# Optimization experiments

Hardware: AMD Instinct MI355X
Metric: run time of the kernel (lower is better)

## Reference

```python
import jax, jax.numpy as jnp
import numpy as np

L_BBOX, L_GIOU, L_OBJ, AUX_W = 5.0, 2.0, 1.0, 0.5
EPS = 1e-7


def _xyxy(b):
    # cxcywh -> xyxy
    return jnp.concatenate([b[..., :2] - b[..., 2:] * 0.5,
                            b[..., :2] + b[..., 2:] * 0.5], axis=-1)


def _giou(a, b):
    # a, b: [..., 4] xyxy (broadcastable) -> giou [...]
    area_a = (a[..., 2] - a[..., 0]) * (a[..., 3] - a[..., 1])
    area_b = (b[..., 2] - b[..., 0]) * (b[..., 3] - b[..., 1])
    lt = jnp.maximum(a[..., :2], b[..., :2])
    rb = jnp.minimum(a[..., 2:], b[..., 2:])
    wh = jnp.maximum(rb - lt, 0.0)
    inter = wh[..., 0] * wh[..., 1]
    union = area_a + area_b - inter
    iou = inter / (union + EPS)
    lte = jnp.minimum(a[..., :2], b[..., :2])
    rbe = jnp.maximum(a[..., 2:], b[..., 2:])
    whe = jnp.maximum(rbe - lte, 0.0)
    enc = whe[..., 0] * whe[..., 1]
    return iou - (enc - union) / (enc + EPS)


def _bce_sum(logits, targets):
    # numerically stable BCE-with-logits, reduction='sum'
    return jnp.sum(jnp.maximum(logits, 0.0) - logits * targets
                   + jnp.log1p(jnp.exp(-jnp.abs(logits))))


def _hungarian(cost):
    # exact Kuhn-Munkres (shortest augmenting path), rectangular, minimization
    cost = np.asarray(cost, dtype=np.float64)
    transposed = cost.shape[0] > cost.shape[1]
    if transposed:
        cost = cost.T
    n, m = cost.shape
    u = np.zeros(n + 1)
    v = np.zeros(m + 1)
    p = np.zeros(m + 1, dtype=np.int64)
    way = np.zeros(m + 1, dtype=np.int64)
    for i in range(1, n + 1):
        p[0] = i
        j0 = 0
        minv = np.full(m + 1, np.inf)
        used = np.zeros(m + 1, dtype=bool)
        while True:
            used[j0] = True
            i0 = p[j0]
            cur = cost[i0 - 1] - u[i0] - v[1:]
            free = ~used[1:]
            better = free & (cur < minv[1:])
            minv[1:] = np.where(better, cur, minv[1:])
            way[1:] = np.where(better, j0, way[1:])
            free_idx = np.nonzero(free)[0]
            jbest = free_idx[np.argmin(minv[1:][free_idx])]
            delta = minv[1 + jbest]
            u[p[used]] += delta
            v[used] -= delta
            minv[~used] -= delta
            j0 = jbest + 1
            if p[j0] == 0:
                break
        while j0:
            j1 = way[j0]
            p[j0] = p[j1]
            j0 = j1
    rows = p[1:] - 1
    cols = np.nonzero(rows >= 0)[0]
    rows = rows[cols]
    if transposed:
        rows, cols = cols, rows
    return rows.astype(np.int64), cols.astype(np.int64)


def _match(pred_bboxes, target_bboxes, bbox_mask):
    # batched cost matrix built on-device, Hungarian per sample (no_grad path)
    pxy = _xyxy(pred_bboxes)
    txy = _xyxy(target_bboxes)
    c_l1 = jnp.sum(jnp.abs(pred_bboxes[:, :, None, :] - target_bboxes[:, None, :, :]), -1)
    c_giou = -_giou(pxy[:, :, None, :], txy[:, None, :, :])
    C = np.asarray(L_BBOX * c_l1 + L_GIOU * c_giou)        # [B,N,M]
    mask = np.asarray(bbox_mask)
    B, N, M = C.shape
    pidx = np.zeros((B, M), np.int32)
    tidx = np.zeros((B, M), np.int32)
    pm = np.zeros((B, M), np.float32)
    for i in range(B):
        vid = np.nonzero(mask[i] > 0.5)[0]
        k = vid.size
        if k == 0:
            continue
        r, c = _hungarian(C[i][:, vid])
        pidx[i, :k] = r
        tidx[i, :k] = vid[c]
        pm[i, :k] = 1.0
    return jnp.asarray(pidx), jnp.asarray(tidx), jnp.asarray(pm)


def _det_losses(pred_bboxes, obj_logits, target_bboxes, pidx, tidx, pm):
    B, N = pred_bboxes.shape[:2]
    bi = jnp.arange(B)[:, None]
    mp = pred_bboxes[bi, pidx]               # [B,M,4] matched preds (padded)
    mt = target_bboxes[bi, tidx]             # [B,M,4] matched targets
    nb = jnp.maximum(pm.sum(), 1.0)
    bbox_loss = (jnp.abs(mp - mt).sum(-1) * pm).sum() / nb
    giou_loss = ((1.0 - _giou(_xyxy(mp), _xyxy(mt))) * pm).sum() / nb
    obj_t = jnp.zeros((B, N), pred_bboxes.dtype).at[bi, pidx].max(pm)
    obj_loss = _bce_sum(obj_logits[..., 0], obj_t) / (B * N)
    return bbox_loss, giou_loss, obj_loss, obj_t


def _total(cls_logits, label, pred_bboxes, obj_scores, target_bboxes,
           aux_pred_bboxes, aux_obj_scores, pidx, tidx, pm):
    B = cls_logits.shape[0]
    cls_loss = -jax.nn.log_softmax(cls_logits, -1)[jnp.arange(B), label].mean()
    bbox_loss, giou_loss, obj_loss, obj_t = _det_losses(
        pred_bboxes, obj_scores, target_bboxes, pidx, tidx, pm)
    # aux losses, vectorized over L decoder layers
    L = aux_pred_bboxes.shape[0]
    bi = jnp.arange(B)[:, None]
    mpa = aux_pred_bboxes[:, bi, pidx]                      # [L,B,M,4]
    mt = target_bboxes[bi, tidx][None]                      # [1,B,M,4]
    nb = jnp.maximum(pm.sum(), 1.0)
    aux_bbox = (jnp.abs(mpa - mt).sum(-1) * pm[None]).sum() / nb
    aux_giou = ((1.0 - _giou(_xyxy(mpa), _xyxy(mt))) * pm[None]).sum() / nb
    N = pred_bboxes.shape[1]
    aux_obj = _bce_sum(aux_obj_scores[..., 0], obj_t[None]) / (B * N)
    aux_loss = (L_BBOX * aux_bbox + L_GIOU * aux_giou + L_OBJ * aux_obj) * AUX_W / L
    return (cls_loss + L_BBOX * bbox_loss + L_GIOU * giou_loss
            + L_OBJ * obj_loss + aux_loss)


def setup_inputs() -> dict:
    B, N, M, L, C = 32, 300, 60, 5, 1000
    ks = jax.random.split(jax.random.key(0), 9)
    cls_logits = jax.random.normal(ks[0], (B, C), jnp.float32)
    label = jax.random.randint(ks[1], (B,), 0, C)
    pred_bboxes = jax.random.uniform(ks[2], (B, N, 4), jnp.float32)
    obj_scores = jax.random.normal(ks[3], (B, N, 1), jnp.float32)
    cxcy = jax.random.uniform(ks[4], (B, M, 2), jnp.float32, 0.2, 0.8)
    wh = jax.random.uniform(ks[5], (B, M, 2), jnp.float32, 0.05, 0.35)
    target_bboxes = jnp.concatenate([cxcy, wh], -1)
    counts = jax.random.randint(ks[6], (B,), 1, M + 1)
    bbox_mask = (jnp.arange(M)[None, :] < counts[:, None]).astype(jnp.float32)
    aux_pred_bboxes = jax.random.uniform(ks[7], (L, B, N, 4), jnp.float32)
    aux_obj_scores = jax.random.normal(ks[8], (L, B, N, 1), jnp.float32)
    return {"cls_logits": cls_logits, "label": label,
            "pred_bboxes": pred_bboxes, "obj_scores": obj_scores,
            "target_bboxes": target_bboxes, "bbox_mask": bbox_mask,
            "aux_pred_bboxes": aux_pred_bboxes,
            "aux_obj_scores": aux_obj_scores}


def reference(cls_logits, label, pred_bboxes, obj_scores, target_bboxes,
              bbox_mask, aux_pred_bboxes, aux_obj_scores):
    pidx, tidx, pm = _match(pred_bboxes, target_bboxes, bbox_mask)
    return _total(cls_logits, label, pred_bboxes, obj_scores, target_bboxes,
                  aux_pred_bboxes, aux_obj_scores, pidx, tidx, pm)
```

## Files before the change

### kernel.cpp

```cpp
#include <hip/hip_runtime.h>
#include <math.h>

#define BN   32
#define NN   300
#define MM   60
#define LAUX 5
#define CNUM 1000

#define LC_ROWS 53
#define CINF 3.0e38f

#define THR_ROW   1.5f
#define EXB_BATCH 3.0f

#define ACC_CLS   0
#define ACC_OBJ   1
#define ACC_AOBJ  2
#define ACC_BBOX  3
#define ACC_GIOU  4
#define ACC_ABBOX 5
#define ACC_AGIOU 6
#define ACC_NB    7

__device__ float  g_cost[BN * MM * NN + 64];
__device__ double g_acc[8];

__device__ __forceinline__ float giou_box(float ax0, float ay0, float ax1, float ay1,
                                          float bx0, float by0, float bx1, float by1) {
    const float EPS = 1e-7f;
    float area_a = (ax1 - ax0) * (ay1 - ay0);
    float area_b = (bx1 - bx0) * (by1 - by0);
    float ltx = fmaxf(ax0, bx0), lty = fmaxf(ay0, by0);
    float rbx = fminf(ax1, bx1), rby = fminf(ay1, by1);
    float w = fmaxf(rbx - ltx, 0.0f), h = fmaxf(rby - lty, 0.0f);
    float inter = w * h;
    float uni = area_a + area_b - inter;
    float iou = inter / (uni + EPS);
    float ex0 = fminf(ax0, bx0), ey0 = fminf(ay0, by0);
    float ex1 = fmaxf(ax1, bx1), ey1 = fmaxf(ay1, by1);
    float ew = fmaxf(ex1 - ex0, 0.0f), eh = fmaxf(ey1 - ey0, 0.0f);
    float enc = ew * eh;
    return iou - (enc - uni) / (enc + EPS);
}

__device__ __forceinline__ float pair_terms(float4 p, float tx0, float ty0,
                                            float tx1, float ty1,
                                            float t0, float t1, float t2, float t3,
                                            float* gi_out) {
    float l1 = fabsf(p.x - t0) + fabsf(p.y - t1) + fabsf(p.z - t2) + fabsf(p.w - t3);
    *gi_out = giou_box(p.x - p.z * 0.5f, p.y - p.w * 0.5f,
                       p.x + p.z * 0.5f, p.y + p.w * 0.5f, tx0, ty0, tx1, ty1);
    return l1;
}


__device__ __forceinline__ unsigned enc_key(float x, int col) {
    unsigned u = __float_as_uint(x);
    unsigned e = (u & 0x80000000u) ? ~u : (u | 0x80000000u);
    return (e & 0xFFFFFE00u) | (unsigned)col;
}
__device__ __forceinline__ float dec_key(unsigned kk) {
    unsigned e = kk & 0xFFFFFE00u;
    unsigned u = (e & 0x80000000u) ? (e & 0x7FFFFFFFu) : ~e;
    return __uint_as_float(u);
}

__device__ __forceinline__ unsigned wave_min_u32(unsigned k) {
#define WSTEP(C) { unsigned t = (unsigned)__builtin_amdgcn_update_dpp((int)k, (int)k, (C), 0xF, 0xF, false); \
                   k = (t < k) ? t : k; }
    WSTEP(0x111) WSTEP(0x112) WSTEP(0x114) WSTEP(0x118) WSTEP(0x142) WSTEP(0x143)
#undef WSTEP
    return (unsigned)__builtin_amdgcn_readlane((int)k, 63);
}

__device__ __forceinline__ void wave_min_pair(unsigned& a, unsigned& b) {
#define PSTEP(C) { \
    unsigned ta = (unsigned)__builtin_amdgcn_update_dpp((int)a, (int)a, (C), 0xF, 0xF, false); \
    unsigned tb = (unsigned)__builtin_amdgcn_update_dpp((int)b, (int)b, (C), 0xF, 0xF, false); \
    a = (ta < a) ? ta : a; \
    b = (tb < b) ? tb : b; }
    PSTEP(0x111) PSTEP(0x112) PSTEP(0x114) PSTEP(0x118) PSTEP(0x142) PSTEP(0x143)
#undef PSTEP
    a = (unsigned)__builtin_amdgcn_readlane((int)a, 63);
    b = (unsigned)__builtin_amdgcn_readlane((int)b, 63);
}

__device__ __forceinline__ void wave_min2_u32(unsigned& a1, unsigned& a2) {
#define W2STEP(C) { \
    unsigned b1 = (unsigned)__builtin_amdgcn_update_dpp(-1, (int)a1, (C), 0xF, 0xF, false); \
    unsigned b2 = (unsigned)__builtin_amdgcn_update_dpp(-1, (int)a2, (C), 0xF, 0xF, false); \
    unsigned lo = (b1 < a1) ? b1 : a1; \
    unsigned hi = (b1 < a1) ? a1 : b1; \
    unsigned mn = (b2 < a2) ? b2 : a2; \
    a2 = (hi < mn) ? hi : mn; \
    a1 = lo; }
    W2STEP(0x111) W2STEP(0x112) W2STEP(0x114) W2STEP(0x118) W2STEP(0x142) W2STEP(0x143)
#undef W2STEP
    a1 = (unsigned)__builtin_amdgcn_readlane((int)a1, 63);
    a2 = (unsigned)__builtin_amdgcn_readlane((int)a2, 63);
}

__device__ __forceinline__ int sel5i(const int* a, int s) {
    int r = a[0];
    r = (s == 1) ? a[1] : r;
    r = (s == 2) ? a[2] : r;
    r = (s == 3) ? a[3] : r;
    r = (s == 4) ? a[4] : r;
    return r;
}
__device__ __forceinline__ float sel5f(const float* a, int s) {
    float r = a[0];
    r = (s == 1) ? a[1] : r;
    r = (s == 2) ? a[2] : r;
    r = (s == 3) ? a[3] : r;
    r = (s == 4) ? a[4] : r;
    return r;
}
__device__ __forceinline__ int rdlane_i(int x, int l) { return __builtin_amdgcn_readlane(x, l); }
__device__ __forceinline__ float rdlane_f(float x, int l) {
    return __uint_as_float((unsigned)__builtin_amdgcn_readlane(__float_as_int(x), l));
}


__global__ __launch_bounds__(256) void fused_kernel(
    const float* __restrict__ mask, const float* __restrict__ pred,
    const float* __restrict__ tgt, const float* __restrict__ obj,
    const float* __restrict__ auxobj, const float* __restrict__ auxp,
    const float* __restrict__ logits, const int* __restrict__ label)
{
    const int b = blockIdx.x;
    const int tid = threadIdx.x;
    const int lane = tid & 63;
    const int wid = tid >> 6;

    __shared__ __align__(16) float lc[LC_ROWS * NN + 24];
    __shared__ int    claimc[NN];
    __shared__ double wred[28];
    __shared__ float  wmax[4];

    const float* pb = pred + (size_t)b * NN * 4;
    const float* tb = tgt + (size_t)b * MM * 4;
    float* gq = g_cost + (size_t)b * (MM * NN);

    for (int e = tid; e < MM * NN; e += 256) {
        int m = e / NN, n = e - m * NN;
        float4 p = *(const float4*)(pb + n * 4);
        float4 t = *(const float4*)(tb + m * 4);
        float l1 = fabsf(p.x - t.x) + fabsf(p.y - t.y) + fabsf(p.z - t.z) + fabsf(p.w - t.w);
        float gi = giou_box(p.x - p.z * 0.5f, p.y - p.w * 0.5f, p.x + p.z * 0.5f, p.y + p.w * 0.5f,
                            t.x - t.z * 0.5f, t.y - t.w * 0.5f, t.x + t.z * 0.5f, t.y + t.w * 0.5f);
        float cst = 5.0f * l1 - 2.0f * gi;
        if (m < LC_ROWS) lc[e] = cst; else gq[e] = cst;
    }
    for (int c = tid; c < NN; c += 256) claimc[c] = 0x7FFFFFFF;

    double so = 0.0, sa = 0.0;
    for (int i = tid; i < NN; i += 256) {
        float x = obj[(size_t)b * NN + i];
        so += (double)(fmaxf(x, 0.0f) + log1pf(expf(-fabsf(x))));
    }
    for (int i = tid; i < LAUX * NN; i += 256) {
        int l = i / NN, n = i - l * NN;
        float x = auxobj[((size_t)l * BN + b) * NN + n];
        sa += (double)(fmaxf(x, 0.0f) + log1pf(expf(-fabsf(x))));
    }
    const float* lrow = logits + (size_t)b * CNUM;
    float mx = -1e30f;
    for (int c = tid; c < CNUM; c += 256) mx = fmaxf(mx, lrow[c]);
    for (int off = 32; off; off >>= 1) mx = fmaxf(mx, __shfl_down(mx, off, 64));
    if (lane == 0) wmax[wid] = mx;
    __syncthreads();
    mx = fmaxf(fmaxf(wmax[0], wmax[1]), fmaxf(wmax[2], wmax[3]));
    double se = 0.0;
    for (int c = tid; c < CNUM; c += 256) se += exp((double)(lrow[c] - mx));
    for (int off = 32; off; off >>= 1) {
        so += __shfl_down(so, off, 64);
        sa += __shfl_down(sa, off, 64);
        se += __shfl_down(se, off, 64);
    }
    if (lane == 0) { wred[wid * 3] = so; wred[wid * 3 + 1] = sa; wred[wid * 3 + 2] = se; }
    __syncthreads();
    if (tid == 0) {
        double soT = wred[0] + wred[3] + wred[6] + wred[9];
        double saT = wred[1] + wred[4] + wred[7] + wred[10];
        double seT = wred[2] + wred[5] + wred[8] + wred[11];
        atomicAdd(&g_acc[ACC_OBJ], soT);
        atomicAdd(&g_acc[ACC_AOBJ], saT);
        atomicAdd(&g_acc[ACC_CLS], log(seT) + (double)mx - (double)lrow[label[b]]);
    }

#define LOAD_ROW(rv, ri) do { int _r = (ri); \
    if (_r < LC_ROWS) { const int _o = _r * NN + lane; \
        rv[0] = lc[_o]; rv[1] = lc[_o + 64]; rv[2] = lc[_o + 128]; \
        rv[3] = lc[_o + 192]; rv[4] = lc[_o + 256]; \
    } else { const float* _g = gq + (size_t)_r * NN + lane; \
        rv[0] = _g[0]; rv[1] = _g[64]; rv[2] = _g[128]; \
        rv[3] = _g[192]; rv[4] = _g[256]; } } while (0)

    float mval = (lane < MM) ? mask[b * MM + lane] : 0.0f;
    int k = __popcll(__ballot(mval > 0.5f));

    float v[5], minv[5], uc[5];
    int pc[5], way[5];
    int used_inv = 0;
#pragma unroll
    for (int s = 0; s < 5; s++) {
        v[s] = 0.0f; uc[s] = 0.0f; pc[s] = 0; way[s] = 0; minv[s] = CINF;
        if (s * 64 + lane >= NN) used_inv |= 1 << s;
    }

    unsigned rowkey = 0xFFFFFFFFu;
    if (wid == 0 && lane < k) {
        unsigned best = 0xFFFFFFFFu;
        if (lane < LC_ROWS) {
            const float* rp = lc + lane * NN;
            for (int c = 0; c < NN; c += 4) {
                float4 q = *(const float4*)(rp + c);
                unsigned c0 = enc_key(q.x, c);
                unsigned c1 = enc_key(q.y, c + 1);
                unsigned c2 = enc_key(q.z, c + 2);
                unsigned c3 = enc_key(q.w, c + 3);
                unsigned m01 = (c0 < c1) ? c0 : c1;
                unsigned m23 = (c2 < c3) ? c2 : c3;
                unsigned m = (m01 < m23) ? m01 : m23;
                best = (m < best) ? m : best;
            }
        } else {
            const float* rp = gq + (size_t)lane * NN;
            for (int c = 0; c < NN; c += 4) {
                float4 q = *(const float4*)(rp + c);
                unsigned c0 = enc_key(q.x, c);
                unsigned c1 = enc_key(q.y, c + 1);
                unsigned c2 = enc_key(q.z, c + 2);
                unsigned c3 = enc_key(q.w, c + 3);
                unsigned m01 = (c0 < c1) ? c0 : c1;
                unsigned m23 = (c2 < c3) ? c2 : c3;
                unsigned m = (m01 < m23) ? m01 : m23;
                best = (m < best) ? m : best;
            }
        }
        rowkey = best;
    }
    float u_row = dec_key(rowkey);
    int jr = (int)(rowkey & 0x1FFu);
    if (wid == 0 && lane < k) atomicMin(&claimc[jr], lane);
    __syncthreads();

    if (wid == 0) {
        unsigned long long assigned;
        {
            int jrs = (lane < k) ? jr : 0;
            bool won = (lane < k) && (claimc[jrs] == lane);
            assigned = __ballot(won);
        }
#pragma unroll
        for (int s = 0; s < 5; s++) {
            int c = s * 64 + lane;
            int w = (c < NN) ? claimc[c] : 0x7FFFFFFF;
            bool hit = (w != 0x7FFFFFFF);
            int wm = hit ? w : 0;
            unsigned kw = (unsigned)__builtin_amdgcn_ds_bpermute(wm << 2, (int)rowkey);
            float uw = dec_key(kw);
            pc[s] = hit ? (w + 1) : pc[s];
            uc[s] = hit ? uw : uc[s];
        }

        unsigned long long kmask = (k >= 64) ? ~0ull : ((1ull << k) - 1ull);
        unsigned long long pool = ~assigned & kmask;
        unsigned long long leftover = 0ull;
        {
            unsigned long long once = 0ull, twice = 0ull;
            int guard = 0;
            while (pool && guard++ < 4 * MM + 16) {
                int r = (int)__builtin_ctzll(pool);
                pool &= pool - 1;
                if ((twice >> r) & 1ull) { leftover |= 1ull << r; continue; }
                if ((once >> r) & 1ull) twice |= 1ull << r; else once |= 1ull << r;

                float rv[5];
                LOAD_ROW(rv, r);
                unsigned k1 = 0xFFFFFFFFu, k2 = 0xFFFFFFFFu;
#pragma unroll
                for (int s = 0; s < 5; s++) {
                    int c = s * 64 + lane;
                    unsigned kk = ((used_inv >> s) & 1) ? 0xFFFFFFFFu : enc_key(rv[s] - v[s], c);
                    unsigned lo = (kk < k1) ? kk : k1;
                    unsigned hi = (kk < k1) ? k1 : kk;
                    k2 = (hi < k2) ? hi : k2;
                    k1 = lo;
                }
                wave_min2_u32(k1, k2);
                float m1 = dec_key(k1), m2 = dec_key(k2);
                int j1 = (int)(k1 & 0x1FFu);
                int sl = j1 >> 6, ow = j1 & 63;
                int pj = rdlane_i(sel5i(pc, sl), ow);
                float dv = m2 - m1;
                u_row = (lane == r) ? m2 : u_row;
#pragma unroll
                for (int s = 0; s < 5; s++) {
                    bool hit = (lane == ow) && (s == sl);
                    v[s]  = hit ? v[s] - dv : v[s];
                    pc[s] = hit ? r + 1    : pc[s];
                    uc[s] = hit ? m2       : uc[s];
                }
                if (pj > 0) pool |= 1ull << (pj - 1);
            }
            leftover |= pool;
        }

        float exb = EXB_BATCH;
        while (leftover) {
            int r = (int)__builtin_ctzll(leftover);
            leftover &= leftover - 1;

            {
                float rv[5];
                LOAD_ROW(rv, r);
                unsigned kAll = 0xFFFFFFFFu, kFree = 0xFFFFFFFFu;
#pragma unroll
                for (int s = 0; s < 5; s++) {
                    int c = s * 64 + lane;
                    bool valid = !((used_inv >> s) & 1);
                    unsigned kk = valid ? enc_key(rv[s] - v[s], c) : 0xFFFFFFFFu;
                    kAll = (kk < kAll) ? kk : kAll;
                    unsigned kf = (valid && pc[s] == 0) ? kk : 0xFFFFFFFFu;
                    kFree = (kf < kFree) ? kf : kFree;
                }
                wave_min_pair(kAll, kFree);
                float m1 = dec_key(kAll), mf = dec_key(kFree);
                float spend = mf - m1;
                if (spend <= fminf(THR_ROW, exb)) {
                    exb -= spend;
                    int jf = (int)(kFree & 0x1FFu);
                    int slf = jf >> 6, owf = jf & 63;
                    u_row = (lane == r) ? m1 : u_row;
#pragma unroll
                    for (int s = 0; s < 5; s++) {
                        bool hit = (lane == owf) && (s == slf);
                        pc[s] = hit ? r + 1 : pc[s];
                        uc[s] = hit ? m1    : uc[s];
                    }
                    continue;
                }
            }

            int used = used_inv;
#pragma unroll
            for (int s = 0; s < 5; s++) minv[s] = CINF;
            float u_cur = rdlane_f(u_row, r);
            float u_i0 = u_cur;
            int i0 = r + 1;
            int j0 = 0;

            for (int guard = 0; guard < NN + 4; guard++) {
                if (j0 > 0) {
                    int c0 = j0 - 1, ow0 = c0 & 63, sl0 = c0 >> 6;
                    used |= (lane == ow0) ? (1 << sl0) : 0;
                }
                float rv[5];
                LOAD_ROW(rv, i0 - 1);
                unsigned kbest = 0xFFFFFFFFu;
#pragma unroll
                for (int s = 0; s < 5; s++) {
                    int c = s * 64 + lane;
                    bool skip = (used >> s) & 1;
                    float cur = rv[s] - u_i0 - v[s];
                    bool lt = !skip && (cur < minv[s]);
                    minv[s] = lt ? cur : minv[s];
                    way[s]  = lt ? j0 : way[s];
                    unsigned kk = skip ? 0xFFFFFFFFu : enc_key(minv[s], c);
                    kbest = (kk < kbest) ? kk : kbest;
                }
                unsigned kmin = wave_min_u32(kbest);
                float delta = dec_key(kmin);
                int jb = (int)(kmin & 0x1FFu);

                int sl = jb >> 6, ow = jb & 63;
                int pj = rdlane_i(sel5i(pc, sl), ow);
                float uj = rdlane_f(sel5f(uc, sl), ow);

                u_cur += delta;
#pragma unroll
                for (int s = 0; s < 5; s++) {
                    bool us = (used >> s) & 1;
                    v[s]    = us ? v[s] - delta   : v[s];
                    uc[s]   = us ? uc[s] + delta  : uc[s];
                    minv[s] = us ? minv[s]        : minv[s] - delta;
                }

                j0 = jb + 1;
                if (pj == 0) break;
                i0 = pj;
                u_i0 = uj;
            }

            int j = j0;
            int safety = 0;
            while (j && safety++ < NN + 4) {
                int co = j - 1, ow = co & 63, sl = co >> 6;
                int j1 = rdlane_i(sel5i(way, sl), ow);
                int pnew; float unew;
                if (j1 == 0) { pnew = r + 1; unew = u_cur; }
                else {
                    int co1 = j1 - 1, ow1 = co1 & 63, sl1 = co1 >> 6;
                    pnew = rdlane_i(sel5i(pc, sl1), ow1);
                    unew = rdlane_f(sel5f(uc, sl1), ow1);
                }
#pragma unroll
                for (int s = 0; s < 5; s++) {
                    bool hit = (lane == ow) && (s == sl);
                    pc[s] = hit ? pnew : pc[s];
                    uc[s] = hit ? unew : uc[s];
                }
                j = j1;
            }
        }

#pragma unroll
        for (int s = 0; s < 5; s++) {
            int c = s * 64 + lane;
            if (c < NN) claimc[c] = pc[s] - 1;
        }
    }
    __syncthreads();
#undef LOAD_ROW

    {
        double sb = 0.0, sg = 0.0, sab = 0.0, sag = 0.0, nb = 0.0;
        double som = 0.0, saom = 0.0;
        for (int it = tid; it < NN * (1 + LAUX); it += 256) {
            int l = it / NN, c = it - l * NN;
            int t = claimc[c];
            if (t >= 0) {
                float4 tg = *(const float4*)(tb + t * 4);
                float tx0 = tg.x - tg.z * 0.5f, ty0 = tg.y - tg.w * 0.5f;
                float tx1 = tg.x + tg.z * 0.5f, ty1 = tg.y + tg.w * 0.5f;
                if (l == 0) {
                    float4 p = *(const float4*)(pb + c * 4);
                    float gi;
                    float l1 = pair_terms(p, tx0, ty0, tx1, ty1, tg.x, tg.y, tg.z, tg.w, &gi);
                    sb += (double)l1;
                    sg += (double)(1.0f - gi);
                    nb += 1.0;
                    som += (double)obj[(size_t)b * NN + c];
                } else {
                    int la = l - 1;
                    float4 a = *(const float4*)(auxp + (((size_t)la * BN + b) * NN + c) * 4);
                    float gi;
                    float l1 = pair_terms(a, tx0, ty0, tx1, ty1, tg.x, tg.y, tg.z, tg.w, &gi);
                    sab += (double)l1;
                    sag += (double)(1.0f - gi);
                    saom += (double)auxobj[((size_t)la * BN + b) * NN + c];
                }
            }
        }
        for (int off = 32; off; off >>= 1) {
            sb   += __shfl_down(sb, off, 64);
            sg   += __shfl_down(sg, off, 64);
            sab  += __shfl_down(sab, off, 64);
            sag  += __shfl_down(sag, off, 64);
            nb   += __shfl_down(nb, off, 64);
            som  += __shfl_down(som, off, 64);
            saom += __shfl_down(saom, off, 64);
        }
        if (lane == 0) {
            double* wr = wred + wid * 7;
            wr[0] = sb; wr[1] = sg; wr[2] = sab; wr[3] = sag;
            wr[4] = nb; wr[5] = som; wr[6] = saom;
        }
        __syncthreads();
        if (tid == 0) {
            double tb0 = wred[0] + wred[7] + wred[14] + wred[21];
            double tg0 = wred[1] + wred[8] + wred[15] + wred[22];
            double tab = wred[2] + wred[9] + wred[16] + wred[23];
            double tag = wred[3] + wred[10] + wred[17] + wred[24];
            double tnb = wred[4] + wred[11] + wred[18] + wred[25];
            double tom = wred[5] + wred[12] + wred[19] + wred[26];
            double tam = wred[6] + wred[13] + wred[20] + wred[27];
            atomicAdd(&g_acc[ACC_BBOX], tb0);
            atomicAdd(&g_acc[ACC_GIOU], tg0);
            atomicAdd(&g_acc[ACC_ABBOX], tab);
            atomicAdd(&g_acc[ACC_AGIOU], tag);
            atomicAdd(&g_acc[ACC_NB], tnb);
            atomicAdd(&g_acc[ACC_OBJ], -tom);
            atomicAdd(&g_acc[ACC_AOBJ], -tam);
        }
    }
}

__global__ void final_kernel(float* __restrict__ out) {
    if (threadIdx.x == 0 && blockIdx.x == 0) {
        double nb = g_acc[ACC_NB];
        if (nb < 1.0) nb = 1.0;
        double cls = g_acc[ACC_CLS] / (double)BN;
        double bbox = g_acc[ACC_BBOX] / nb;
        double giou = g_acc[ACC_GIOU] / nb;
        double obj = g_acc[ACC_OBJ] / (double)(BN * NN);
        double ab = g_acc[ACC_ABBOX] / nb;
        double ag = g_acc[ACC_AGIOU] / nb;
        double ao = g_acc[ACC_AOBJ] / (double)(BN * NN);
        double aux = (5.0 * ab + 2.0 * ag + 1.0 * ao) * 0.5 / (double)LAUX;
        out[0] = (float)(cls + 5.0 * bbox + 2.0 * giou + obj + aux);
        for (int i = 0; i < 8; i++) g_acc[i] = 0.0;
    }
}

extern "C" void kernel_launch(void* const* d_in, const int* in_sizes, int n_in,
                              void* d_out, int out_size, void* d_ws, size_t ws_size,
                              hipStream_t stream) {
    const float* cls_logits = (const float*)d_in[0];
    const int* label = (const int*)d_in[1];
    const float* pred_bboxes = (const float*)d_in[2];
    const float* obj_scores = (const float*)d_in[3];
    const float* target_bboxes = (const float*)d_in[4];
    const float* bbox_mask = (const float*)d_in[5];
    const float* aux_pred = (const float*)d_in[6];
    const float* aux_obj = (const float*)d_in[7];
    float* out = (float*)d_out;

    fused_kernel<<<BN, 256, 0, stream>>>(bbox_mask, pred_bboxes, target_bboxes,
                                         obj_scores, aux_obj, aux_pred,
                                         cls_logits, label);
    final_kernel<<<1, 1, 0, stream>>>(out);
}
```

Baseline: 230.5 us.

## Keep full cost matrix in LDS and fold final reduction into main kernel

Enlarges the shared-memory cost buffer to hold all 60 target rows, removing the global-memory spill for the rows past 53 and the branch in every row load of the assignment loop. It also drops the separate finalize kernel: a global done counter lets the last block compute the output and reset the accumulators. This trades a larger LDS allocation and extra atomics for fewer global reads and one less launch.

```diff
diff --git a/kernel.cpp b/kernel.cpp
--- a/kernel.cpp
+++ b/kernel.cpp
@@ -7,7 +7,6 @@
 #define LAUX 5
 #define CNUM 1000
 
-#define LC_ROWS 53
 #define CINF 3.0e38f
 
 #define THR_ROW   1.5f
@@ -22,8 +21,8 @@
 #define ACC_AGIOU 6
 #define ACC_NB    7
 
-__device__ float  g_cost[BN * MM * NN + 64];
-__device__ double g_acc[8];
+__device__ double   g_acc[8];
+__device__ unsigned g_done = 0;
 
 __device__ __forceinline__ float giou_box(float ax0, float ay0, float ax1, float ay1,
                                           float bx0, float by0, float bx1, float by1) {
@@ -126,21 +125,21 @@
     const float* __restrict__ mask, const float* __restrict__ pred,
     const float* __restrict__ tgt, const float* __restrict__ obj,
     const float* __restrict__ auxobj, const float* __restrict__ auxp,
-    const float* __restrict__ logits, const int* __restrict__ label)
+    const float* __restrict__ logits, const int* __restrict__ label,
+    float* __restrict__ out)
 {
     const int b = blockIdx.x;
     const int tid = threadIdx.x;
     const int lane = tid & 63;
     const int wid = tid >> 6;
 
-    __shared__ __align__(16) float lc[LC_ROWS * NN + 24];
+    __shared__ __align__(16) float lc[MM * NN + 24];
     __shared__ int    claimc[NN];
     __shared__ double wred[28];
     __shared__ float  wmax[4];
 
     const float* pb = pred + (size_t)b * NN * 4;
     const float* tb = tgt + (size_t)b * MM * 4;
-    float* gq = g_cost + (size_t)b * (MM * NN);
 
     for (int e = tid; e < MM * NN; e += 256) {
         int m = e / NN, n = e - m * NN;
@@ -149,8 +148,7 @@
         float l1 = fabsf(p.x - t.x) + fabsf(p.y - t.y) + fabsf(p.z - t.z) + fabsf(p.w - t.w);
         float gi = giou_box(p.x - p.z * 0.5f, p.y - p.w * 0.5f, p.x + p.z * 0.5f, p.y + p.w * 0.5f,
                             t.x - t.z * 0.5f, t.y - t.w * 0.5f, t.x + t.z * 0.5f, t.y + t.w * 0.5f);
-        float cst = 5.0f * l1 - 2.0f * gi;
-        if (m < LC_ROWS) lc[e] = cst; else gq[e] = cst;
+        lc[e] = 5.0f * l1 - 2.0f * gi;
     }
     for (int c = tid; c < NN; c += 256) claimc[c] = 0x7FFFFFFF;
 
@@ -189,13 +187,9 @@
         atomicAdd(&g_acc[ACC_CLS], log(seT) + (double)mx - (double)lrow[label[b]]);
     }
 
-#define LOAD_ROW(rv, ri) do { int _r = (ri); \
-    if (_r < LC_ROWS) { const int _o = _r * NN + lane; \
-        rv[0] = lc[_o]; rv[1] = lc[_o + 64]; rv[2] = lc[_o + 128]; \
-        rv[3] = lc[_o + 192]; rv[4] = lc[_o + 256]; \
-    } else { const float* _g = gq + (size_t)_r * NN + lane; \
-        rv[0] = _g[0]; rv[1] = _g[64]; rv[2] = _g[128]; \
-        rv[3] = _g[192]; rv[4] = _g[256]; } } while (0)
+#define LOAD_ROW(rv, ri) do { const int _o = (ri) * NN + lane; \
+    rv[0] = lc[_o]; rv[1] = lc[_o + 64]; rv[2] = lc[_o + 128]; \
+    rv[3] = lc[_o + 192]; rv[4] = lc[_o + 256]; } while (0)
 
     float mval = (lane < MM) ? mask[b * MM + lane] : 0.0f;
     int k = __popcll(__ballot(mval > 0.5f));
@@ -212,32 +206,17 @@
     unsigned rowkey = 0xFFFFFFFFu;
     if (wid == 0 && lane < k) {
         unsigned best = 0xFFFFFFFFu;
-        if (lane < LC_ROWS) {
-            const float* rp = lc + lane * NN;
-            for (int c = 0; c < NN; c += 4) {
-                float4 q = *(const float4*)(rp + c);
-                unsigned c0 = enc_key(q.x, c);
-                unsigned c1 = enc_key(q.y, c + 1);
-                unsigned c2 = enc_key(q.z, c + 2);
-                unsigned c3 = enc_key(q.w, c + 3);
-                unsigned m01 = (c0 < c1) ? c0 : c1;
-                unsigned m23 = (c2 < c3) ? c2 : c3;
-                unsigned m = (m01 < m23) ? m01 : m23;
-                best = (m < best) ? m : best;
-            }
-        } else {
-            const float* rp = gq + (size_t)lane * NN;
-            for (int c = 0; c < NN; c += 4) {
-                float4 q = *(const float4*)(rp + c);
-                unsigned c0 = enc_key(q.x, c);
-                unsigned c1 = enc_key(q.y, c + 1);
-                unsigned c2 = enc_key(q.z, c + 2);
-                unsigned c3 = enc_key(q.w, c + 3);
-                unsigned m01 = (c0 < c1) ? c0 : c1;
-                unsigned m23 = (c2 < c3) ? c2 : c3;
-                unsigned m = (m01 < m23) ? m01 : m23;
-                best = (m < best) ? m : best;
-            }
+        const float* rp = lc + lane * NN;
+        for (int c = 0; c < NN; c += 4) {
+            float4 q = *(const float4*)(rp + c);
+            unsigned c0 = enc_key(q.x, c);
+            unsigned c1 = enc_key(q.y, c + 1);
+            unsigned c2 = enc_key(q.z, c + 2);
+            unsigned c3 = enc_key(q.w, c + 3);
+            unsigned m01 = (c0 < c1) ? c0 : c1;
+            unsigned m23 = (c2 < c3) ? c2 : c3;
+            unsigned m = (m01 < m23) ? m01 : m23;
+            best = (m < best) ? m : best;
         }
         rowkey = best;
     }
@@ -484,24 +463,29 @@
             atomicAdd(&g_acc[ACC_NB], tnb);
             atomicAdd(&g_acc[ACC_OBJ], -tom);
             atomicAdd(&g_acc[ACC_AOBJ], -tam);
-        }
-    }
-}
-
-__global__ void final_kernel(float* __restrict__ out) {
-    if (threadIdx.x == 0 && blockIdx.x == 0) {
-        double nb = g_acc[ACC_NB];
-        if (nb < 1.0) nb = 1.0;
-        double cls = g_acc[ACC_CLS] / (double)BN;
-        double bbox = g_acc[ACC_BBOX] / nb;
-        double giou = g_acc[ACC_GIOU] / nb;
-        double obj = g_acc[ACC_OBJ] / (double)(BN * NN);
-        double ab = g_acc[ACC_ABBOX] / nb;
-        double ag = g_acc[ACC_AGIOU] / nb;
-        double ao = g_acc[ACC_AOBJ] / (double)(BN * NN);
-        double aux = (5.0 * ab + 2.0 * ag + 1.0 * ao) * 0.5 / (double)LAUX;
-        out[0] = (float)(cls + 5.0 * bbox + 2.0 * giou + obj + aux);
-        for (int i = 0; i < 8; i++) g_acc[i] = 0.0;
+
+            __threadfence();
+            unsigned old = atomicAdd(&g_done, 1u);
+            if (old == BN - 1) {
+                double acc[8];
+                for (int i = 0; i < 8; i++)
+                    acc[i] = atomicAdd(&g_acc[i], 0.0);
+                double nbv = acc[ACC_NB];
+                if (nbv < 1.0) nbv = 1.0;
+                double cls = acc[ACC_CLS] / (double)BN;
+                double bbox = acc[ACC_BBOX] / nbv;
+                double giou = acc[ACC_GIOU] / nbv;
+                double objv = acc[ACC_OBJ] / (double)(BN * NN);
+                double ab = acc[ACC_ABBOX] / nbv;
+                double ag = acc[ACC_AGIOU] / nbv;
+                double ao = acc[ACC_AOBJ] / (double)(BN * NN);
+                double aux = (5.0 * ab + 2.0 * ag + 1.0 * ao) * 0.5 / (double)LAUX;
+                out[0] = (float)(cls + 5.0 * bbox + 2.0 * giou + objv + aux);
+                for (int i = 0; i < 8; i++)
+                    atomicExch((unsigned long long*)&g_acc[i], 0ull);
+                atomicExch(&g_done, 0u);
+            }
+        }
     }
 }
 
@@ -520,6 +504,5 @@
 
     fused_kernel<<<BN, 256, 0, stream>>>(bbox_mask, pred_bboxes, target_bboxes,
                                          obj_scores, aux_obj, aux_pred,
-                                         cls_logits, label);
-    final_kernel<<<1, 1, 0, stream>>>(out);
-}
+                                         cls_logits, label, out);
+}
```

Measured after the change: 204.3 us, median of 2. -11.4%, faster.
